# Optimization experiments

Hardware: AMD Instinct MI355X
Metric: run time of the kernel (lower is better)

The kernel has to match this reference:

```python
import jax, jax.numpy as jnp
import numpy as np

B, S, H = 2, 2048, 2048
E = 4
I = 8192
EI = I // E  # expert intermediate size
VOCAB = 100000

def setup_inputs() -> dict:
    key = jax.random.key(0)
    k1, k2, k3, k4, k5 = jax.random.split(key, 5)
    hidden_states = jax.random.normal(k1, (B, S, H), dtype=jnp.float32)
    token_ids = jax.random.randint(k2, (B, S), 0, VOCAB, dtype=jnp.int64)
    gate_proj = jax.random.normal(k3, (E, H, EI), dtype=jnp.float32) * 0.02
    up_proj = jax.random.normal(k4, (E, H, EI), dtype=jnp.float32) * 0.02
    down_proj = jax.random.normal(k5, (E, EI, H), dtype=jnp.float32) * 0.02
    return {"hidden_states": hidden_states, "token_ids": token_ids,
            "gate_proj": gate_proj, "up_proj": up_proj, "down_proj": down_proj}

def reference(hidden_states, token_ids, gate_proj, up_proj, down_proj):
    b, s, h = hidden_states.shape
    e_dim = gate_proj.shape[0]
    # token_to_expert = arange(vocab) % E  (no frequency table)
    tid = jnp.clip(token_ids, 0, VOCAB - 1)
    expert_ids = (tid % e_dim).reshape(-1)          # [T]
    x = hidden_states.reshape(-1, h)                # [T, H]
    T = x.shape[0]
    t_idx = jnp.arange(T)
    # grouped GEMM == per-token GEMM with token's expert weight; compute per-expert then select
    gate_all = jnp.einsum('td,edf->tef', x, gate_proj)   # [T, E, EI]
    up_all = jnp.einsum('td,edf->tef', x, up_proj)       # [T, E, EI]
    gate = gate_all[t_idx, expert_ids]                   # [T, EI]
    up = up_all[t_idx, expert_ids]                       # [T, EI]
    inter = jax.nn.silu(gate) * up                       # fused SwiGLU
    out_all = jnp.einsum('tf,efd->ted', inter, down_proj)  # [T, E, H]
    out = out_all[t_idx, expert_ids]                     # [T, H]
    return out.reshape(b, s, h)
```

## Files before the change

### kernel.cpp

```cpp
#include <hip/hip_runtime.h>

#define H_DIM 2048
#define EI_DIM 2048
#define NEXP 4
#define BM 144
#define SEG 1152
#define NROWS 4608
#define NTM 32
#define NKB 64
#define NB 16
#define AFRAG 576
#define WFRAG 512

typedef __attribute__((ext_vector_type(4))) float f32x4;
typedef __attribute__((ext_vector_type(8))) short bf16x8;
typedef __attribute__((ext_vector_type(4))) short bf16x4;
typedef __attribute__((ext_vector_type(4))) int i32x4;

__device__ __forceinline__ short f2bf(float f) {
  unsigned u = __builtin_bit_cast(unsigned, f);
  u += 0x7fffu + ((u >> 16) & 1u);
  return (short)(u >> 16);
}

__device__ __forceinline__ unsigned pkbf(float lo, float hi) {
  unsigned r;
  asm("v_cvt_pk_bf16_f32 %0, %1, %2" : "=v"(r) : "v"(lo), "v"(hi));
  return r;
}

__device__ __forceinline__ void gload16(const void* g, void* l) {
  __builtin_amdgcn_global_load_lds(
      (const __attribute__((address_space(1))) unsigned*)g,
      (__attribute__((address_space(3))) unsigned*)l, 16, 0, 0);
}

__global__ void route_kernel(const void* __restrict__ token_ids,
                             int* __restrict__ meta, int* __restrict__ row2tok) {
  __shared__ unsigned long long wtot[4];
  const int tid = threadIdx.x;
  const int lane = tid & 63;
  const int wv = tid >> 6;

  for (int i = tid; i < NROWS; i += 256) row2tok[i] = -1;

  const int* ti32 = (const int*)token_ids;
  bool is64 = true;
  for (int i = 0; i < 16; ++i)
    if (ti32[2 * i + 1] != 0) is64 = false;

  const int base = tid * 16;
  unsigned long long pack = 0ULL;
  unsigned eps = 0;
  for (int i = 0; i < 16; ++i) {
    long long v = is64 ? ((const long long*)token_ids)[base + i]
                       : (long long)ti32[base + i];
    if (v < 0) v = 0;
    if (v > 99999) v = 99999;
    int e = (int)(v & 3);
    eps |= (unsigned)e << (2 * i);
    pack += 1ULL << (16 * e);
  }

  unsigned long long incl = pack;
  for (int off = 1; off < 64; off <<= 1) {
    unsigned long long up = __shfl_up(incl, off, 64);
    if (lane >= off) incl += up;
  }
  if (lane == 63) wtot[wv] = incl;
  __syncthreads();

  unsigned long long waveBase = 0;
  for (int w = 0; w < 4; ++w)
    if (w < wv) waveBase += wtot[w];
  const unsigned long long exclu = waveBase + incl - pack;

  if (tid == 0) {
    meta[0] = 36;
    for (int t = 0; t < 36; ++t) meta[1 + t] = t / 9;
  }

  int cur[4];
  for (int e = 0; e < 4; ++e)
    cur[e] = e * SEG + (int)((exclu >> (16 * e)) & 0xffff);
  for (int i = 0; i < 16; ++i) {
    int e = (int)((eps >> (2 * i)) & 3);
    int idx = cur[e]++;
    if (idx < (e + 1) * SEG) row2tok[idx] = base + i;
  }
}


__global__ __launch_bounds__(256) void convert_gather_kernel(
    const float* __restrict__ gW, const float* __restrict__ uW,
    const float* __restrict__ dW, const float* __restrict__ hidden,
    const int* __restrict__ row2tok, short* __restrict__ Pg,
    short* __restrict__ Pu, short* __restrict__ Pd, short* __restrict__ xp) {
  __shared__ float Lf[2][2048];
  const int b = blockIdx.x;
  const int tid = threadIdx.x;

  if (b >= 3072) {
    const int gb = b - 3072;
    const int tile = gb >> 6;
    const int kb = gb & 63;
    short* db = xp + ((size_t)tile * NKB + kb) * (AFRAG * 8);
#pragma unroll
    for (int q = 0; q < 3; ++q) {
      if (q == 2 && tid >= 64) break;
      const int idx = q * 256 + tid;
      const int ks = idx / 144, r = idx - ks * 144;
      const int tok = row2tok[tile * BM + r];
      bf16x8 v = {0, 0, 0, 0, 0, 0, 0, 0};
      if (tok >= 0) {
        const f32x4* s =
            (const f32x4*)(hidden + (size_t)tok * H_DIM + kb * 32 + ks * 8);
        f32x4 a = s[0], bb = s[1];
        v[0] = f2bf(a[0]); v[1] = f2bf(a[1]); v[2] = f2bf(a[2]); v[3] = f2bf(a[3]);
        v[4] = f2bf(bb[0]); v[5] = f2bf(bb[1]); v[6] = f2bf(bb[2]); v[7] = f2bf(bb[3]);
      }
      *(bf16x8*)(db + idx * 8) = v;
    }
    return;
  }

  const int mat = b >> 10;
  const int r10 = b & 1023;
  const int e = r10 >> 8;
  const int kb = (r10 >> 3) & 31;
  const int ks = r10 & 7;
  const float* src = mat == 0 ? gW : (mat == 1 ? uW : dW);
  short* dst = mat == 0 ? Pg : (mat == 1 ? Pu : Pd);

  const int lr = tid >> 5;
  const int lc = (tid & 31) * 8;
  const int wbase = lr * 256 + (lc ^ ((lr & 1) << 2));

  const float* lp = src + ((size_t)e * 2048 + kb * 64 + ks * 8 + lr) * 2048 + lc;
  short* doutB = dst + (size_t)(e * 512 + kb) * 8192 + (ks * 128) * 8;

  f32x4 r0[2], r1[2];
  r0[0] = __builtin_nontemporal_load((const f32x4*)lp);
  r1[0] = __builtin_nontemporal_load((const f32x4*)(lp + 4));

#pragma unroll
  for (int q = 0; q < 8; ++q) {
    const int s = q & 1;
    *(f32x4*)&Lf[s][wbase] = r0[s];
    *(f32x4*)&Lf[s][wbase ^ 4] = r1[s];
    if (q < 7) {
      const float* np = lp + (q + 1) * 256;
      r0[s ^ 1] = __builtin_nontemporal_load((const f32x4*)np);
      r1[s ^ 1] = __builtin_nontemporal_load((const f32x4*)(np + 4));
    }
    asm volatile("s_waitcnt lgkmcnt(0)" ::: "memory");
    __builtin_amdgcn_s_barrier();
    __builtin_amdgcn_sched_barrier(0);
    float v[8];
#pragma unroll
    for (int j = 0; j < 8; ++j)
      v[j] = Lf[s][(j * 256 + tid) ^ ((j & 1) << 2)];
    i32x4 w;
    w[0] = pkbf(v[0], v[1]); w[1] = pkbf(v[2], v[3]);
    w[2] = pkbf(v[4], v[5]); w[3] = pkbf(v[6], v[7]);
    const int c = q * 256 + tid;
    const int nb2 = c >> 7, cc = c & 127;
    *(i32x4*)(doutB + (size_t)nb2 * (32 * 8192) + cc * 8) = w;
    asm volatile("s_waitcnt lgkmcnt(0)" ::: "memory");
    __builtin_amdgcn_s_barrier();
    __builtin_amdgcn_sched_barrier(0);
  }
}

__global__ __launch_bounds__(256, 2) void gemm1_kernel(
    const short* __restrict__ xp, const short* __restrict__ Pg,
    const short* __restrict__ Pu, short* __restrict__ inter) {
  const int b0 = blockIdx.x;
  const int swz = (b0 & 7) * 64 + (b0 >> 3);
  const int tile = swz >> 4, nb = swz & 15;
  const int e = tile >> 3;

  __shared__ short L[3][12800];

  const int tid = threadIdx.x, lane = tid & 63, wv = tid >> 6;
  const int l15 = lane & 15, lks = lane >> 4;
  const int wuni = (tid & 192) * 16;

  f32x4 accG[9][2] = {};
  f32x4 accU[9][2] = {};

  const short* aB = xp + (size_t)(tile * NKB) * (AFRAG * 8);
  const short* gB = Pg + (size_t)((e * NB + nb) * NKB) * (WFRAG * 8);
  const short* uB = Pu + (size_t)((e * NB + nb) * NKB) * (WFRAG * 8);

#define STAGE1(kb, bf)                                                        \
  {                                                                           \
    const short* a = aB + (size_t)(kb) * (AFRAG * 8);                         \
    const short* g = gB + (size_t)(kb) * (WFRAG * 8);                         \
    const short* u = uB + (size_t)(kb) * (WFRAG * 8);                         \
    char* la = (char*)&L[bf][0];                                              \
    char* lg = (char*)&L[bf][4608];                                           \
    char* lu = (char*)&L[bf][8704];                                           \
    gload16(a + tid * 8, la + wuni);                                          \
    gload16(a + (256 + tid) * 8, la + 4096 + wuni);                           \
    if (lane < 16)                                                            \
      gload16(a + (512 + wv * 16 + lane) * 8, la + 8192 + wv * 256);          \
    gload16(g + tid * 8, lg + wuni);                                          \
    gload16(g + (256 + tid) * 8, lg + 4096 + wuni);                           \
    gload16(u + tid * 8, lu + wuni);                                          \
    gload16(u + (256 + tid) * 8, lu + 4096 + wuni);                           \
  }

  STAGE1(0, 0);
  STAGE1(1, 1);

  int bcur = 0;
  for (int kb = 0; kb < NKB; ++kb) {
    if (kb < NKB - 1)
      asm volatile("s_waitcnt vmcnt(7)" ::: "memory");
    else
      asm volatile("s_waitcnt vmcnt(0)" ::: "memory");
    __builtin_amdgcn_s_barrier();
    __builtin_amdgcn_sched_barrier(0);
    if (kb < NKB - 2) {
      int bn2 = bcur + 2;
      if (bn2 >= 3) bn2 -= 3;
      STAGE1(kb + 2, bn2);
    }
    const short* As = &L[bcur][0];
    const short* Gs = &L[bcur][4608];
    const short* Us = &L[bcur][8704];
    bf16x8 af[9], bg[2], bu[2];
#pragma unroll
    for (int m = 0; m < 9; ++m)
      af[m] = *(const bf16x8*)(As + (lks * 144 + m * 16 + l15) * 8);
#pragma unroll
    for (int n = 0; n < 2; ++n) {
      const int c = wv * 32 + n * 16 + l15;
      bg[n] = *(const bf16x8*)(Gs + (lks * 128 + c) * 8);
      bu[n] = *(const bf16x8*)(Us + (lks * 128 + c) * 8);
    }
    __builtin_amdgcn_s_setprio(1);
#pragma unroll
    for (int m = 0; m < 9; ++m)
#pragma unroll
      for (int n = 0; n < 2; ++n) {
        accG[m][n] = __builtin_amdgcn_mfma_f32_16x16x32_bf16(
            af[m], bg[n], accG[m][n], 0, 0, 0);
        accU[m][n] = __builtin_amdgcn_mfma_f32_16x16x32_bf16(
            af[m], bu[n], accU[m][n], 0, 0, 0);
      }
    __builtin_amdgcn_s_setprio(0);
    if (++bcur == 3) bcur = 0;
  }
#undef STAGE1

#pragma unroll
  for (int n = 0; n < 2; ++n) {
    const int C = nb * 128 + wv * 32 + n * 16 + l15;
    const int kb2 = C >> 5, ks2 = (C >> 3) & 3, kj = C & 7;
    short* ib = inter + (((size_t)tile * NKB + kb2) * AFRAG + ks2 * 144) * 8 + kj;
#pragma unroll
    for (int m = 0; m < 9; ++m)
#pragma unroll
      for (int j = 0; j < 4; ++j) {
        const int r = m * 16 + (lks << 2) + j;
        const float g = accG[m][n][j], u = accU[m][n][j];
        const float s = g / (1.0f + __expf(-g));
        ib[(size_t)r * 8] = f2bf(s * u);
      }
  }
}

__global__ __launch_bounds__(256, 2) void gemm2_kernel(
    const short* __restrict__ inter, const short* __restrict__ Pd,
    const int* __restrict__ row2tok, float* __restrict__ out) {
  const int b0 = blockIdx.x;
  const int swz = (b0 & 7) * 64 + (b0 >> 3);
  const int tile = swz >> 4, nb = swz & 15;
  const int e = tile >> 3;

  __shared__ short L[3][8704];

  const int tid = threadIdx.x, lane = tid & 63, wv = tid >> 6;
  const int l15 = lane & 15, lks = lane >> 4;
  const int wuni = (tid & 192) * 16;

  f32x4 acc[9][2] = {};

  const short* aB = inter + (size_t)(tile * NKB) * (AFRAG * 8);
  const short* dB = Pd + (size_t)((e * NB + nb) * NKB) * (WFRAG * 8);

#define STAGE2(kb, bf)                                                        \
  {                                                                           \
    const short* a = aB + (size_t)(kb) * (AFRAG * 8);                         \
    const short* d = dB + (size_t)(kb) * (WFRAG * 8);                         \
    char* la = (char*)&L[bf][0];                                              \
    char* ld = (char*)&L[bf][4608];                                           \
    gload16(a + tid * 8, la + wuni);                                          \
    gload16(a + (256 + tid) * 8, la + 4096 + wuni);                           \
    if (lane < 16)                                                            \
      gload16(a + (512 + wv * 16 + lane) * 8, la + 8192 + wv * 256);          \
    gload16(d + tid * 8, ld + wuni);                                          \
    gload16(d + (256 + tid) * 8, ld + 4096 + wuni);                           \
  }

  STAGE2(0, 0);
  STAGE2(1, 1);

  int bcur = 0;
  for (int kb = 0; kb < NKB; ++kb) {
    if (kb < NKB - 1)
      asm volatile("s_waitcnt vmcnt(5)" ::: "memory");
    else
      asm volatile("s_waitcnt vmcnt(0)" ::: "memory");
    __builtin_amdgcn_s_barrier();
    __builtin_amdgcn_sched_barrier(0);
    if (kb < NKB - 2) {
      int bn2 = bcur + 2;
      if (bn2 >= 3) bn2 -= 3;
      STAGE2(kb + 2, bn2);
    }
    const short* As = &L[bcur][0];
    const short* Bs = &L[bcur][4608];
    bf16x8 af[9], bd[2];
#pragma unroll
    for (int m = 0; m < 9; ++m)
      af[m] = *(const bf16x8*)(As + (lks * 144 + m * 16 + l15) * 8);
#pragma unroll
    for (int n = 0; n < 2; ++n)
      bd[n] = *(const bf16x8*)(Bs + (lks * 128 + wv * 32 + n * 16 + l15) * 8);
    __builtin_amdgcn_s_setprio(1);
#pragma unroll
    for (int m = 0; m < 9; ++m)
#pragma unroll
      for (int n = 0; n < 2; ++n)
        acc[m][n] = __builtin_amdgcn_mfma_f32_16x16x32_bf16(af[m], bd[n],
                                                            acc[m][n], 0, 0, 0);
    __builtin_amdgcn_s_setprio(0);
    if (++bcur == 3) bcur = 0;
  }
#undef STAGE2

#pragma unroll
  for (int m = 0; m < 9; ++m)
#pragma unroll
    for (int j = 0; j < 4; ++j) {
      const int r = tile * BM + m * 16 + (lks << 2) + j;
      const int tok = row2tok[r];
      if (tok >= 0) {
        float* orow = out + (size_t)tok * H_DIM + nb * 128 + wv * 32 + l15;
#pragma unroll
        for (int n = 0; n < 2; ++n) orow[n * 16] = acc[m][n][j];
      }
    }
}


__global__ void gather_fb_kernel(const float* __restrict__ hidden,
                                 const int* __restrict__ row2tok,
                                 short* __restrict__ xperm) {
  const int r = blockIdx.x;
  const int tok = row2tok[r];
  const int tid = threadIdx.x;
  f32x4 a = {0.f, 0.f, 0.f, 0.f}, b = {0.f, 0.f, 0.f, 0.f};
  if (tok >= 0) {
    const f32x4* src = (const f32x4*)(hidden + (size_t)tok * H_DIM + 8 * tid);
    a = src[0];
    b = src[1];
  }
  bf16x8 v;
  v[0] = f2bf(a[0]); v[1] = f2bf(a[1]); v[2] = f2bf(a[2]); v[3] = f2bf(a[3]);
  v[4] = f2bf(b[0]); v[5] = f2bf(b[1]); v[6] = f2bf(b[2]); v[7] = f2bf(b[3]);
  *(bf16x8*)(xperm + (size_t)r * H_DIM + 8 * tid) = v;
}

__global__ __launch_bounds__(256, 2) void gemm1_fb_kernel(
    const short* __restrict__ xperm, const float* __restrict__ gateW,
    const float* __restrict__ upW, const int* __restrict__ meta,
    short* __restrict__ inter) {
  const int tm = blockIdx.x;
  if (tm >= meta[0]) return;
  const int e = meta[1 + tm];
  const int rowBase = tm * 128;
  const int colBase = blockIdx.y * 128;
  const float* gW = gateW + (size_t)e * H_DIM * EI_DIM;
  const float* uW = upW + (size_t)e * H_DIM * EI_DIM;

  __shared__ short As[128 * 64];
  __shared__ short Bg[128 * 64];
  __shared__ short Bu[128 * 64];

  const int tid = threadIdx.x;
  const int lane = tid & 63;
  const int wv = tid >> 6;
  const int wr = (wv >> 1) * 64;
  const int wc = (wv & 1) * 64;

  f32x4 accG[4][4] = {};
  f32x4 accU[4][4] = {};

  const int ar = tid >> 3;
  const int ak = (tid & 7) * 8;
  const int bn = (tid & 31) * 4;
  const int bk = (tid >> 5) * 4;

  for (int k0 = 0; k0 < H_DIM; k0 += 64) {
    bf16x8 av[4];
#pragma unroll
    for (int p = 0; p < 4; ++p) {
      int r = ar + p * 32;
      av[p] = *(const bf16x8*)(xperm + (size_t)(rowBase + r) * H_DIM + k0 + ak);
    }
    f32x4 gv[2][4], uv[2][4];
#pragma unroll
    for (int p = 0; p < 2; ++p) {
      int kk = k0 + bk + p * 32;
#pragma unroll
      for (int i = 0; i < 4; ++i) {
        gv[p][i] = *(const f32x4*)(gW + (size_t)(kk + i) * EI_DIM + colBase + bn);
        uv[p][i] = *(const f32x4*)(uW + (size_t)(kk + i) * EI_DIM + colBase + bn);
      }
    }
    __syncthreads();
#pragma unroll
    for (int p = 0; p < 4; ++p) {
      int r = ar + p * 32;
      int idx = (r * 64 + ak) ^ ((r & 7) << 3);
      *(bf16x8*)(As + idx) = av[p];
    }
#pragma unroll
    for (int p = 0; p < 2; ++p) {
      int kk = bk + p * 32;
#pragma unroll
      for (int j = 0; j < 4; ++j) {
        int rowp = bn + j;
        int idx = (rowp * 64 + kk) ^ ((rowp & 7) << 3);
        bf16x4 vg, vu;
        vg[0] = f2bf(gv[p][0][j]); vg[1] = f2bf(gv[p][1][j]);
        vg[2] = f2bf(gv[p][2][j]); vg[3] = f2bf(gv[p][3][j]);
        vu[0] = f2bf(uv[p][0][j]); vu[1] = f2bf(uv[p][1][j]);
        vu[2] = f2bf(uv[p][2][j]); vu[3] = f2bf(uv[p][3][j]);
        *(bf16x4*)(Bg + idx) = vg;
        *(bf16x4*)(Bu + idx) = vu;
      }
    }
    __syncthreads();
#pragma unroll
    for (int kk = 0; kk < 64; kk += 32) {
      const int kb = kk + ((lane >> 4) << 3);
      bf16x8 af[4], bgf[4], buf_[4];
#pragma unroll
      for (int m = 0; m < 4; ++m) {
        int r = wr + m * 16 + (lane & 15);
        af[m] = *(const bf16x8*)(As + ((r * 64 + kb) ^ ((r & 7) << 3)));
      }
#pragma unroll
      for (int n = 0; n < 4; ++n) {
        int c = wc + n * 16 + (lane & 15);
        int idx = (c * 64 + kb) ^ ((c & 7) << 3);
        bgf[n] = *(const bf16x8*)(Bg + idx);
        buf_[n] = *(const bf16x8*)(Bu + idx);
      }
#pragma unroll
      for (int m = 0; m < 4; ++m)
#pragma unroll
        for (int n = 0; n < 4; ++n) {
          accG[m][n] = __builtin_amdgcn_mfma_f32_16x16x32_bf16(
              af[m], bgf[n], accG[m][n], 0, 0, 0);
          accU[m][n] = __builtin_amdgcn_mfma_f32_16x16x32_bf16(
              af[m], buf_[n], accU[m][n], 0, 0, 0);
        }
    }
  }
#pragma unroll
  for (int m = 0; m < 4; ++m)
#pragma unroll
    for (int n = 0; n < 4; ++n) {
      int c = colBase + wc + n * 16 + (lane & 15);
#pragma unroll
      for (int j = 0; j < 4; ++j) {
        int r = rowBase + wr + m * 16 + ((lane >> 4) << 2) + j;
        float g = accG[m][n][j], u = accU[m][n][j];
        float s = g / (1.0f + __expf(-g));
        inter[(size_t)r * EI_DIM + c] = f2bf(s * u);
      }
    }
}

__global__ __launch_bounds__(256, 2) void gemm2_fb_kernel(
    const short* __restrict__ inter, const float* __restrict__ downW,
    const int* __restrict__ meta, const int* __restrict__ row2tok,
    float* __restrict__ out) {
  const int tm = blockIdx.x;
  if (tm >= meta[0]) return;
  const int e = meta[1 + tm];
  const int rowBase = tm * 128;
  const int colBase = blockIdx.y * 128;
  const float* dW = downW + (size_t)e * EI_DIM * H_DIM;

  __shared__ short As[128 * 64];
  __shared__ short Bs[128 * 64];

  const int tid = threadIdx.x;
  const int lane = tid & 63;
  const int wv = tid >> 6;
  const int wr = (wv >> 1) * 64;
  const int wc = (wv & 1) * 64;

  f32x4 acc[4][4] = {};

  const int ar = tid >> 3;
  const int ak = (tid & 7) * 8;
  const int bn = (tid & 31) * 4;
  const int bk = (tid >> 5) * 4;

  for (int k0 = 0; k0 < EI_DIM; k0 += 64) {
    bf16x8 av[4];
#pragma unroll
    for (int p = 0; p < 4; ++p) {
      int r = ar + p * 32;
      av[p] = *(const bf16x8*)(inter + (size_t)(rowBase + r) * EI_DIM + k0 + ak);
    }
    f32x4 dv[2][4];
#pragma unroll
    for (int p = 0; p < 2; ++p) {
      int kk = k0 + bk + p * 32;
#pragma unroll
      for (int i = 0; i < 4; ++i)
        dv[p][i] = *(const f32x4*)(dW + (size_t)(kk + i) * H_DIM + colBase + bn);
    }
    __syncthreads();
#pragma unroll
    for (int p = 0; p < 4; ++p) {
      int r = ar + p * 32;
      int idx = (r * 64 + ak) ^ ((r & 7) << 3);
      *(bf16x8*)(As + idx) = av[p];
    }
#pragma unroll
    for (int p = 0; p < 2; ++p) {
      int kk = bk + p * 32;
#pragma unroll
      for (int j = 0; j < 4; ++j) {
        int rowp = bn + j;
        int idx = (rowp * 64 + kk) ^ ((rowp & 7) << 3);
        bf16x4 vd;
        vd[0] = f2bf(dv[p][0][j]); vd[1] = f2bf(dv[p][1][j]);
        vd[2] = f2bf(dv[p][2][j]); vd[3] = f2bf(dv[p][3][j]);
        *(bf16x4*)(Bs + idx) = vd;
      }
    }
    __syncthreads();
#pragma unroll
    for (int kk = 0; kk < 64; kk += 32) {
      const int kb = kk + ((lane >> 4) << 3);
      bf16x8 af[4], bf_[4];
#pragma unroll
      for (int m = 0; m < 4; ++m) {
        int r = wr + m * 16 + (lane & 15);
        af[m] = *(const bf16x8*)(As + ((r * 64 + kb) ^ ((r & 7) << 3)));
      }
#pragma unroll
      for (int n = 0; n < 4; ++n) {
        int c = wc + n * 16 + (lane & 15);
        bf_[n] = *(const bf16x8*)(Bs + ((c * 64 + kb) ^ ((c & 7) << 3)));
      }
#pragma unroll
      for (int m = 0; m < 4; ++m)
#pragma unroll
        for (int n = 0; n < 4; ++n)
          acc[m][n] = __builtin_amdgcn_mfma_f32_16x16x32_bf16(
              af[m], bf_[n], acc[m][n], 0, 0, 0);
    }
  }
#pragma unroll
  for (int m = 0; m < 4; ++m)
#pragma unroll
    for (int j = 0; j < 4; ++j) {
      int r = rowBase + wr + m * 16 + ((lane >> 4) << 2) + j;
      int tok = row2tok[r];
      if (tok >= 0) {
        float* orow = out + (size_t)tok * H_DIM + colBase + wc + (lane & 15);
#pragma unroll
        for (int n = 0; n < 4; ++n) orow[n * 16] = acc[m][n][j];
      }
    }
}


extern "C" void kernel_launch(void* const* d_in, const int* in_sizes, int n_in,
                              void* d_out, int out_size, void* d_ws,
                              size_t ws_size, hipStream_t stream) {
  const float* hidden = (const float*)d_in[0];
  const void* token_ids = d_in[1];
  const float* gateW = (const float*)d_in[2];
  const float* upW = (const float*)d_in[3];
  const float* downW = (const float*)d_in[4];
  float* out = (float*)d_out;

  int* meta = (int*)d_ws;
  int* row2tok = meta + 64;

  const size_t wMatShorts = (size_t)NEXP * NB * 32 * 8192;
  const size_t xpShorts = (size_t)NTM * NKB * AFRAG * 8;
  const size_t need = 32768 + 3 * wMatShorts * 2 + 2 * xpShorts * 2;

  route_kernel<<<1, 256, 0, stream>>>(token_ids, meta, row2tok);

  if (ws_size >= need) {
    short* Pg = (short*)((char*)d_ws + 32768);
    short* Pu = Pg + wMatShorts;
    short* Pd = Pu + wMatShorts;
    short* xp = Pd + wMatShorts;
    short* inter = xp + xpShorts;

    convert_gather_kernel<<<5120, 256, 0, stream>>>(
        gateW, upW, downW, hidden, row2tok, Pg, Pu, Pd, xp);
    gemm1_kernel<<<512, 256, 0, stream>>>(xp, Pg, Pu, inter);
    gemm2_kernel<<<512, 256, 0, stream>>>(inter, Pd, row2tok, out);
  } else {
    short* xperm = (short*)((char*)d_ws + 32768);
    short* inter = xperm + (size_t)NROWS * H_DIM;

    gather_fb_kernel<<<NROWS, 256, 0, stream>>>(hidden, row2tok, xperm);
    gemm1_fb_kernel<<<dim3(36, EI_DIM / 128), 256, 0, stream>>>(
        xperm, gateW, upW, meta, inter);
    gemm2_fb_kernel<<<dim3(36, H_DIM / 128), 256, 0, stream>>>(
        inter, downW, meta, row2tok, out);
  }
}
```

Baseline: 177.0 us.

## Move down-projection weight conversion into gemm1 to overlap with compute

The fp32-to-bf16 repacking of the down-projection weights moves out of the standalone convert kernel and into the gemm1 main loop. Each gemm1 block converts a share of the tiles every fourth k-iteration, hiding that memory-bound work behind the MFMA compute. This shrinks the convert grid from 5120 to 4096 blocks. The cost is extra global loads and stores inside the gemm1 loop, which may disturb its vmcnt-based pipelining and add register pressure.

```diff
diff --git a/kernel.cpp b/kernel.cpp
--- a/kernel.cpp
+++ b/kernel.cpp
@@ -35,6 +35,28 @@
       (__attribute__((address_space(3))) unsigned*)l, 16, 0, 0);
 }
 
+__device__ __forceinline__ void produce_wtile(const float* __restrict__ W,
+                                              short* __restrict__ P, int e,
+                                              int nb, int kb, int tid) {
+  const int c = tid & 127;
+  const int ksh = tid >> 7;
+  const float* sb = W + ((size_t)e * 2048 + kb * 32) * 2048 + nb * 128 + c;
+  short* db = P + ((size_t)((e * 16 + nb) * 64 + kb)) * 4096 + c * 8;
+#pragma unroll
+  for (int k2 = 0; k2 < 2; ++k2) {
+    const int ks = ksh * 2 + k2;
+    const float* s = sb + (size_t)(ks * 8) * 2048;
+    float v[8];
+#pragma unroll
+    for (int j = 0; j < 8; ++j)
+      v[j] = __builtin_nontemporal_load(s + (size_t)j * 2048);
+    i32x4 w;
+    w[0] = pkbf(v[0], v[1]); w[1] = pkbf(v[2], v[3]);
+    w[2] = pkbf(v[4], v[5]); w[3] = pkbf(v[6], v[7]);
+    *(i32x4*)(db + ks * 1024) = w;
+  }
+}
+
 __global__ void route_kernel(const void* __restrict__ token_ids,
                              int* __restrict__ meta, int* __restrict__ row2tok) {
   __shared__ unsigned long long wtot[4];
@@ -93,15 +115,14 @@
 
 __global__ __launch_bounds__(256) void convert_gather_kernel(
     const float* __restrict__ gW, const float* __restrict__ uW,
-    const float* __restrict__ dW, const float* __restrict__ hidden,
-    const int* __restrict__ row2tok, short* __restrict__ Pg,
-    short* __restrict__ Pu, short* __restrict__ Pd, short* __restrict__ xp) {
+    const float* __restrict__ hidden, const int* __restrict__ row2tok,
+    short* __restrict__ Pg, short* __restrict__ Pu, short* __restrict__ xp) {
   __shared__ float Lf[2][2048];
   const int b = blockIdx.x;
   const int tid = threadIdx.x;
 
-  if (b >= 3072) {
-    const int gb = b - 3072;
+  if (b >= 2048) {
+    const int gb = b - 2048;
     const int tile = gb >> 6;
     const int kb = gb & 63;
     short* db = xp + ((size_t)tile * NKB + kb) * (AFRAG * 8);
@@ -129,8 +150,8 @@
   const int e = r10 >> 8;
   const int kb = (r10 >> 3) & 31;
   const int ks = r10 & 7;
-  const float* src = mat == 0 ? gW : (mat == 1 ? uW : dW);
-  short* dst = mat == 0 ? Pg : (mat == 1 ? Pu : Pd);
+  const float* src = mat == 0 ? gW : uW;
+  short* dst = mat == 0 ? Pg : Pu;
 
   const int lr = tid >> 5;
   const int lc = (tid & 31) * 8;
@@ -174,11 +195,13 @@
 
 __global__ __launch_bounds__(256, 2) void gemm1_kernel(
     const short* __restrict__ xp, const short* __restrict__ Pg,
-    const short* __restrict__ Pu, short* __restrict__ inter) {
+    const short* __restrict__ Pu, const float* __restrict__ dW,
+    short* __restrict__ Pd, short* __restrict__ inter) {
   const int b0 = blockIdx.x;
   const int swz = (b0 & 7) * 64 + (b0 >> 3);
   const int tile = swz >> 4, nb = swz & 15;
   const int e = tile >> 3;
+  const int e2 = b0 >> 7, nb2 = (b0 >> 3) & 15, g8 = b0 & 7;
 
   __shared__ short L[3][12800];
 
@@ -222,6 +245,10 @@
       asm volatile("s_waitcnt vmcnt(0)" ::: "memory");
     __builtin_amdgcn_s_barrier();
     __builtin_amdgcn_sched_barrier(0);
+    if ((kb & 3) == 0 && kb >= 4 && kb <= 32) {
+      produce_wtile(dW, Pd, e2, nb2, g8 * 8 + ((kb >> 2) - 1), tid);
+      __builtin_amdgcn_sched_barrier(0);
+    }
     if (kb < NKB - 2) {
       int bn2 = bcur + 2;
       if (bn2 >= 3) bn2 -= 3;
@@ -614,9 +641,9 @@
     short* xp = Pd + wMatShorts;
     short* inter = xp + xpShorts;
 
-    convert_gather_kernel<<<5120, 256, 0, stream>>>(
-        gateW, upW, downW, hidden, row2tok, Pg, Pu, Pd, xp);
-    gemm1_kernel<<<512, 256, 0, stream>>>(xp, Pg, Pu, inter);
+    convert_gather_kernel<<<4096, 256, 0, stream>>>(gateW, upW, hidden,
+                                                    row2tok, Pg, Pu, xp);
+    gemm1_kernel<<<512, 256, 0, stream>>>(xp, Pg, Pu, downW, Pd, inter);
     gemm2_kernel<<<512, 256, 0, stream>>>(inter, Pd, row2tok, out);
   } else {
     short* xperm = (short*)((char*)d_ws + 32768);
```

Result: faster. 170.5 us, median of 2 (-3.6%).
